# Kernel optimization log

Hardware: AMD Instinct MI355X
Metric: run time of the kernel (lower is better)

The kernel has to match this reference:

```python
import jax, jax.numpy as jnp
import numpy as np

B, T, C, H = 2, 2048, 1024, 16
D = C // H  # d_head = 64


def setup_inputs() -> dict:
    key = jax.random.key(0)
    k1, k2, k3 = jax.random.split(key, 3)
    x = jax.random.normal(k1, (B, T, C), dtype=jnp.float32)
    # torch Linear weights stored pre-transposed as [in, out] so we apply x @ W
    w_qkv = jax.random.normal(k2, (C, 3 * C), dtype=jnp.float32) * (C ** -0.5)
    w_out = jax.random.normal(k3, (C, C), dtype=jnp.float32) * (C ** -0.5)
    charge_w = jnp.array([0.0, 3.0, 6.0], dtype=jnp.float32)  # CHARGES init
    # causal mask, broadcast over batch and heads; mask==0 positions are blocked
    mask = jnp.tril(jnp.ones((1, 1, T, T), dtype=jnp.int32))
    return {"x": x, "mask": mask, "w_qkv": w_qkv, "w_out": w_out, "charge_w": charge_w}


def reference(x, mask, w_qkv, w_out, charge_w):
    B, T, C = x.shape
    H = 16
    D = C // H
    qkv = (x @ w_qkv).reshape(B, T, 3, H, D)
    q, k, v = qkv[:, :, 0], qkv[:, :, 1], qkv[:, :, 2]  # each [B,T,H,D]
    scale = D ** -0.5
    attn = jnp.einsum("bqhd,bkhd->bhqk", q, k) * scale  # [B,H,T,T]
    charge_bias = jnp.mod(jnp.sum(charge_w), 9.0) * 0.001  # scalar bias
    attn = attn + charge_bias
    attn = jnp.where(mask == 0, jnp.float32(-1e9), attn)
    attn = jax.nn.softmax(attn, axis=-1)  # dropout is identity in eval mode
    out = jnp.einsum("bhqk,bkhd->bqhd", attn, v).reshape(B, T, C)
    return out @ w_out
```

## Files before the change

kernel.cpp:

```cpp
#include <hip/hip_runtime.h>
#include <stdint.h>


typedef __attribute__((ext_vector_type(4))) float f32x4;
typedef __attribute__((ext_vector_type(16))) float f32x16;
typedef __attribute__((ext_vector_type(8))) __bf16 bf16x8;
typedef __attribute__((ext_vector_type(8))) unsigned short ushort8;
typedef __attribute__((ext_vector_type(4))) unsigned short ushort4v;
typedef __attribute__((ext_vector_type(4))) unsigned int uint4v;

#define DEV __device__ __forceinline__

DEV unsigned short f32_to_bf16(float f) {
    union { float f; unsigned int u; } cv; cv.f = f;
    unsigned int u = cv.u;
    return (unsigned short)((u + 0x7FFFu + ((u >> 16) & 1u)) >> 16);
}

DEV float bf16_to_f32(unsigned short u) {
    union { unsigned int i; float f; } cv; cv.i = ((unsigned int)u) << 16;
    return cv.f;
}

DEV bf16x8 load_bf16x8(const unsigned short* p) {
    ushort8 v = *(const ushort8*)p;
    return __builtin_bit_cast(bf16x8, v);
}

DEV unsigned cvt_pk_bf16(float lo, float hi) {
    unsigned r;
    asm("v_cvt_pk_bf16_f32 %0, %1, %2" : "=v"(r) : "v"(lo), "v"(hi));
    return r;
}

DEV void gload_lds16(const void* g, void* l) {
    __builtin_amdgcn_global_load_lds(
        (const __attribute__((address_space(1))) unsigned int*)g,
        (__attribute__((address_space(3))) unsigned int*)l, 16, 0, 0);
}

DEV f32x16 vzero16() {
    f32x16 v;
#pragma unroll
    for (int i = 0; i < 16; ++i) v[i] = 0.f;
    return v;
}

DEV float tmax32(const f32x16& a, const f32x16& b) {
    float m[16];
#pragma unroll
    for (int i = 0; i < 16; ++i) m[i] = fmaxf(a[i], b[i]);
#pragma unroll
    for (int st = 8; st > 0; st >>= 1)
#pragma unroll
        for (int i = 0; i < 8; ++i) if (i < st) m[i] = fmaxf(m[i], m[i + st]);
    return m[0];
}
DEV float tsum32(const f32x16& a, const f32x16& b) {
    float m[16];
#pragma unroll
    for (int i = 0; i < 16; ++i) m[i] = a[i] + b[i];
#pragma unroll
    for (int st = 8; st > 0; st >>= 1)
#pragma unroll
        for (int i = 0; i < 8; ++i) if (i < st) m[i] = m[i] + m[i + st];
    return m[0];
}

__device__ __constant__ unsigned char qQ[32]  = { 6, 5,14,14,14,13, 9, 9, 4,13,13,12,12, 8, 8,15,15,15,15,12,11,11,11,10, 7, 7, 3,10,10, 2, 1, 0};
__device__ __constant__ unsigned char tsQ[32] = { 0, 0, 0,10,20, 0, 0,10, 0,10,19, 0, 9, 0, 9, 0, 8,16,24,18, 0, 8,16, 0, 0, 8, 0, 8,15, 0, 0, 0};
__device__ __constant__ unsigned char teQ[32] = {14,12,10,20,30,10,10,20,10,19,28, 9,18, 9,18, 8,16,24,32,26, 8,16,24, 8, 8,16, 8,15,22, 6, 4, 2};
__device__ __constant__ unsigned char mlQ[32] = {255,255, 4, 5, 6, 7,19,20,255, 8, 9,10,11,21,22, 0, 1, 2, 3,12,13,14,15,16,23,24,255,17,18,255,255,255};
__device__ __constant__ unsigned char obQ[32] = {255,255,255, 3, 4,255,255,13,255, 5, 6,255, 7,255,14,255, 0, 1, 2, 8,255, 9,10,255,255,15,255,11,12,255,255,255};
__device__ __constant__ unsigned char ncs[9]  = {4,3,3,3,3,3,2,2,2};
__device__ __constant__ unsigned char mlbs[9] = {0,4,7,10,13,16,19,21,23};
__device__ __constant__ unsigned char obbs[9] = {0,3,5,7,9,11,13,14,15};

__global__ __launch_bounds__(256) void prep_kernel(const float* __restrict__ x,
                                                   const float* __restrict__ w_qkv,
                                                   const float* __restrict__ w_out,
                                                   unsigned short* __restrict__ xb,
                                                   unsigned short* __restrict__ wqkvT,
                                                   unsigned short* __restrict__ woutT) {
    __shared__ float tl[32][33];
    const int bx = blockIdx.x;
    const int tid = threadIdx.x;
    if (bx < 2048) {
        int i = (bx * 256 + tid) * 8;
        f32x4 a = *(const f32x4*)(x + i);
        f32x4 b = *(const f32x4*)(x + i + 4);
        ushort8 o;
        o[0] = f32_to_bf16(a[0]); o[1] = f32_to_bf16(a[1]);
        o[2] = f32_to_bf16(a[2]); o[3] = f32_to_bf16(a[3]);
        o[4] = f32_to_bf16(b[0]); o[5] = f32_to_bf16(b[1]);
        o[6] = f32_to_bf16(b[2]); o[7] = f32_to_bf16(b[3]);
        *(ushort8*)(xb + i) = o;
        return;
    }
    const float* in;
    unsigned short* out;
    int R, Cn, c0, r0;
    if (bx < 5120) {
        int idx = bx - 2048;
        in = w_qkv; out = wqkvT; R = 1024; Cn = 3072;
        c0 = (idx % 96) * 32; r0 = (idx / 96) * 32;
    } else {
        int idx = bx - 5120;
        in = w_out; out = woutT; R = 1024; Cn = 1024;
        c0 = (idx % 32) * 32; r0 = (idx / 32) * 32;
    }
    const int tx = tid & 31, ty = tid >> 5;
#pragma unroll
    for (int rr = 0; rr < 4; ++rr) {
        int r = ty + rr * 8;
        tl[r][tx] = in[(size_t)(r0 + r) * Cn + c0 + tx];
    }
    __syncthreads();
#pragma unroll
    for (int rr = 0; rr < 4; ++rr) {
        int cc = ty + rr * 8;
        out[(size_t)(c0 + cc) * R + r0 + tx] = f32_to_bf16(tl[tx][cc]);
    }
}

template<bool OUT_BF16, bool SCALE_Q>
__global__ __launch_bounds__(256) void gemm_kernel(
    const unsigned short* __restrict__ A,
    const unsigned short* __restrict__ Bt,
    void* __restrict__ C, int K, int ldc)
{
    __shared__ __align__(16) unsigned short As[3][4096];
    __shared__ __align__(16) unsigned short Bs[3][4096];

    const int tid = threadIdx.x;
    const int lane = tid & 63;
    const int w = tid >> 6;
    const int wr = w >> 1, wc = w & 1;
    const int g = lane >> 4, ci = lane & 15;
    const int bx = blockIdx.x, by = blockIdx.y;
    const int soff = w * 1024 + lane * 16;
    const int srow = soff >> 6;
    const int scch = (soff >> 4) & 3;

#define GSTAGE(buf, k0_) do { \
    _Pragma("unroll") for (int i_ = 0; i_ < 2; ++i_) { \
        int row_ = srow + i_ * 64; \
        gload_lds16(A  + (size_t)(by * 128 + row_) * K + (k0_) + scch * 8, \
                    (char*)As[buf] + i_ * 4096 + w * 1024); \
        gload_lds16(Bt + (size_t)(bx * 128 + row_) * K + (k0_) + scch * 8, \
                    (char*)Bs[buf] + i_ * 4096 + w * 1024); } } while (0)

    f32x4 acc[4][4];
#pragma unroll
    for (int i = 0; i < 4; ++i)
#pragma unroll
        for (int j = 0; j < 4; ++j) acc[i][j] = f32x4{0.f, 0.f, 0.f, 0.f};

    const int nk = K >> 5;
    GSTAGE(0, 0);
    GSTAGE(1, 32);
    asm volatile("s_waitcnt vmcnt(4)" ::: "memory");
    __builtin_amdgcn_sched_barrier(0);
    __builtin_amdgcn_s_barrier();
    __builtin_amdgcn_sched_barrier(0);

    for (int kt = 0; kt < nk; ++kt) {
        const int cur = kt % 3;
        if (kt + 2 < nk) GSTAGE((kt + 2) % 3, (kt + 2) << 5);

        bf16x8 af[4], bfr[4];
#pragma unroll
        for (int mf = 0; mf < 4; ++mf) af[mf]  = load_bf16x8(&As[cur][(wr * 64 + mf * 16 + ci) * 32 + g * 8]);
#pragma unroll
        for (int nf = 0; nf < 4; ++nf) bfr[nf] = load_bf16x8(&Bs[cur][(wc * 64 + nf * 16 + ci) * 32 + g * 8]);
        __builtin_amdgcn_s_setprio(1);
#pragma unroll
        for (int mf = 0; mf < 4; ++mf)
#pragma unroll
            for (int nf = 0; nf < 4; ++nf)
                acc[mf][nf] = __builtin_amdgcn_mfma_f32_16x16x32_bf16(af[mf], bfr[nf], acc[mf][nf], 0, 0, 0);
        __builtin_amdgcn_s_setprio(0);

        if (kt + 2 < nk) asm volatile("s_waitcnt vmcnt(4) lgkmcnt(0)" ::: "memory");
        else             asm volatile("s_waitcnt vmcnt(0) lgkmcnt(0)" ::: "memory");
        __builtin_amdgcn_sched_barrier(0);
        __builtin_amdgcn_s_barrier();
        __builtin_amdgcn_sched_barrier(0);
    }
#undef GSTAGE

#pragma unroll
    for (int mf = 0; mf < 4; ++mf)
#pragma unroll
        for (int nf = 0; nf < 4; ++nf)
#pragma unroll
            for (int r = 0; r < 4; ++r) {
                int row = by * 128 + wr * 64 + mf * 16 + g * 4 + r;
                int col = bx * 128 + wc * 64 + nf * 16 + ci;
                float v = acc[mf][nf][r];
                if (SCALE_Q && col < 1024) v *= 0.1803368801f;
                if (OUT_BF16)
                    ((unsigned short*)C)[(size_t)row * ldc + col] = f32_to_bf16(v);
                else
                    ((float*)C)[(size_t)row * ldc + col] = v;
            }
}

__global__ __launch_bounds__(256) void attn7_kernel(const unsigned short* __restrict__ qkv,
                                                    unsigned short* __restrict__ attn,
                                                    unsigned short* __restrict__ Obuf,
                                                    float* __restrict__ mlbuf) {
    constexpr int T = 2048, HD3 = 3072, Cc = 1024;
    __shared__ __align__(16) unsigned short Ks[3][4096];
    __shared__ __align__(16) unsigned short Vt[2][4096];

    const int tid = threadIdx.x;
    const int lane = tid & 63;
    const int w = tid >> 6;
    const int l31 = lane & 31;
    const int hi = lane >> 5;

    const int bx = blockIdx.x;
    const int j = bx >> 5;
    const int bh = bx & 31;
    const int q = qQ[j];
    const int ts = tsQ[j], te = teQ[j];
    const int h = bh & 15;
    const int b = bh >> 4;
    const int q0w = q * 128 + w * 32;
    const int qrow = q0w + l31;
    const size_t base = (size_t)b * T * HD3;
    const int ntc = te - ts;

    bf16x8 qf[4];
#pragma unroll
    for (int t = 0; t < 4; ++t)
        qf[t] = load_bf16x8(qkv + base + (size_t)qrow * HD3 + h * 64 + t * 16 + hi * 8);

    f32x16 acc0 = vzero16(), acc1 = vzero16();
    float m = -3e38f, l = 0.f;

    ushort8 vA0, vA1, vB0, vB1;
#define LOADV(tile, r0, r1) do { int kv0_ = (tile) * 64; \
    int rr0_ = tid >> 3, cc0_ = tid & 7; \
    r0 = *(const ushort8*)(qkv + base + (size_t)(kv0_ + rr0_) * HD3 + 2 * Cc + h * 64 + cc0_ * 8); \
    int c1_ = 256 + tid; int rr1_ = c1_ >> 3, cc1_ = c1_ & 7; \
    r1 = *(const ushort8*)(qkv + base + (size_t)(kv0_ + rr1_) * HD3 + 2 * Cc + h * 64 + cc1_ * 8); } while (0)

#define DMAK(tile, kb) do { int kv0_ = (tile) * 64; \
    _Pragma("unroll") for (int i_ = 0; i_ < 2; ++i_) { \
        int off_ = i_ * 4096 + w * 1024 + lane * 16; \
        int row_ = off_ >> 7; \
        int csw_ = ((lane & 7) * 8) ^ ((row_ & 7) * 8); \
        gload_lds16(qkv + base + (size_t)(kv0_ + row_) * HD3 + Cc + h * 64 + csw_, \
                    (void*)(((char*)&Ks[kb][0]) + i_ * 4096 + w * 1024)); } } while (0)

#define WRITEV(vb, r0, r1) do { \
    _Pragma("unroll") for (int i_ = 0; i_ < 2; ++i_) { \
        int c_ = i_ * 256 + tid; int row_ = c_ >> 3, cc_ = c_ & 7; \
        ushort8 v_ = i_ ? r1 : r0; \
        _Pragma("unroll") for (int j_ = 0; j_ < 8; ++j_) { \
            int d_ = cc_ * 8 + j_; \
            int sw_ = ((d_ ^ (d_ >> 3)) & 7) * 8; \
            Vt[vb][d_ * 64 + (row_ ^ sw_)] = v_[j_]; } } } while (0)

    LOADV(ts, vA0, vA1);
    DMAK(ts, 0);
    asm volatile("s_waitcnt vmcnt(0)" ::: "memory");
    __builtin_amdgcn_sched_barrier(0);
    WRITEV(0, vA0, vA1);
    LOADV(ts + 1, vB0, vB1);
    DMAK(ts + 1, 1);
    asm volatile("s_waitcnt lgkmcnt(0)" ::: "memory");
    __builtin_amdgcn_sched_barrier(0);
    __builtin_amdgcn_s_barrier();
    __builtin_amdgcn_sched_barrier(0);

    for (int tt = 0; tt < ntc; ++tt) {
        const int t = ts + tt;
        const int kv0 = t * 64;
        const int kcur = tt % 3;
        const int vcur = tt & 1;
        const bool act = (kv0 <= q0w + 31);
        const bool pre2 = (tt + 2) < ntc;

        if (tt + 1 < ntc) {
            if (tt & 1) WRITEV(vcur ^ 1, vA0, vA1); else WRITEV(vcur ^ 1, vB0, vB1);
        }
        if (pre2) {
            if (tt & 1) LOADV(t + 2, vB0, vB1); else LOADV(t + 2, vA0, vA1);
            DMAK(t + 2, (tt + 2) % 3);
        }

        if (act) {
            f32x16 s0 = vzero16(), s1 = vzero16();
            bf16x8 pf[4];
            const bool st1_ok = (kv0 + 32 <= q0w + 31);
            __builtin_amdgcn_s_setprio(1);
#pragma unroll
            for (int tf = 0; tf < 4; ++tf) {
                int row = l31;
                int idx = kcur * 4096 + row * 64 + ((tf * 16 + hi * 8) ^ ((row & 7) * 8));
                s0 = __builtin_amdgcn_mfma_f32_32x32x16_bf16(load_bf16x8(&Ks[0][idx]), qf[tf], s0, 0, 0, 0);
            }
            if (st1_ok) {
#pragma unroll
                for (int tf = 0; tf < 4; ++tf) {
                    int row = 32 + l31;
                    int idx = kcur * 4096 + row * 64 + ((tf * 16 + hi * 8) ^ ((row & 7) * 8));
                    s1 = __builtin_amdgcn_mfma_f32_32x32x16_bf16(load_bf16x8(&Ks[0][idx]), qf[tf], s1, 0, 0, 0);
                }
            }
            __builtin_amdgcn_s_setprio(0);
            const bool needmask = (kv0 + 63 > q0w);
            if (needmask) {
#pragma unroll
                for (int G = 0; G < 4; ++G)
#pragma unroll
                    for (int rr = 0; rr < 4; ++rr) {
                        int kvb = kv0 + 8 * G + 4 * hi + rr;
                        s0[G * 4 + rr] = (kvb      <= qrow) ? s0[G * 4 + rr] : -3e38f;
                        s1[G * 4 + rr] = (kvb + 32 <= qrow) ? s1[G * 4 + rr] : -3e38f;
                    }
            }
            float pmax = tmax32(s0, s1);
            pmax = fmaxf(pmax, __shfl_xor(pmax, 32));
            if (!__all(pmax - m <= 11.5f)) {
                float mnew = fmaxf(m, pmax);
                float alpha = exp2f(m - mnew);
                m = mnew;
                l *= alpha;
#pragma unroll
                for (int i = 0; i < 16; ++i) { acc0[i] *= alpha; acc1[i] *= alpha; }
            }
#pragma unroll
            for (int i = 0; i < 16; ++i) {
                s0[i] = exp2f(s0[i] - m);
                s1[i] = exp2f(s1[i] - m);
            }

            unsigned pk0[4][2], pk1[4][2];
#pragma unroll
            for (int G = 0; G < 4; ++G) {
                pk0[G][0] = cvt_pk_bf16(s0[G * 4 + 0], s0[G * 4 + 1]);
                pk0[G][1] = cvt_pk_bf16(s0[G * 4 + 2], s0[G * 4 + 3]);
                pk1[G][0] = cvt_pk_bf16(s1[G * 4 + 0], s1[G * 4 + 1]);
                pk1[G][1] = cvt_pk_bf16(s1[G * 4 + 2], s1[G * 4 + 3]);
            }
#pragma unroll
            for (int tf = 0; tf < 4; ++tf) {
                const int kb = tf & 1;
                unsigned sA0, sA1, sB0, sB1;
                if (tf < 2) { sA0 = pk0[2 * kb][0]; sA1 = pk0[2 * kb][1]; sB0 = pk0[2 * kb + 1][0]; sB1 = pk0[2 * kb + 1][1]; }
                else        { sA0 = pk1[2 * kb][0]; sA1 = pk1[2 * kb][1]; sB0 = pk1[2 * kb + 1][0]; sB1 = pk1[2 * kb + 1][1]; }
                unsigned sd0 = hi ? sA0 : sB0, sd1 = hi ? sA1 : sB1;
                unsigned rc0 = (unsigned)__shfl_xor((int)sd0, 32);
                unsigned rc1 = (unsigned)__shfl_xor((int)sd1, 32);
                uint4v u;
                u[0] = hi ? rc0 : sA0;  u[1] = hi ? rc1 : sA1;
                u[2] = hi ? sB0 : rc0;  u[3] = hi ? sB1 : rc1;
                pf[tf] = __builtin_bit_cast(bf16x8, u);
            }

            __builtin_amdgcn_s_setprio(1);
#pragma unroll
            for (int tf = 0; tf < 4; ++tf) {
                {
                    int d = l31, sw = ((d ^ (d >> 3)) & 7) * 8;
                    bf16x8 vf = load_bf16x8(&Vt[vcur][d * 64 + ((tf * 16 + hi * 8) ^ sw)]);
                    acc0 = __builtin_amdgcn_mfma_f32_32x32x16_bf16(vf, pf[tf], acc0, 0, 0, 0);
                }
                {
                    int d = 32 + l31, sw = ((d ^ (d >> 3)) & 7) * 8;
                    bf16x8 vf = load_bf16x8(&Vt[vcur][d * 64 + ((tf * 16 + hi * 8) ^ sw)]);
                    acc1 = __builtin_amdgcn_mfma_f32_32x32x16_bf16(vf, pf[tf], acc1, 0, 0, 0);
                }
            }
            __builtin_amdgcn_s_setprio(0);

            float rsum = tsum32(s0, s1);
            l += rsum + __shfl_xor(rsum, 32);
        }

        if (pre2) asm volatile("s_waitcnt vmcnt(4) lgkmcnt(0)" ::: "memory");
        else      asm volatile("s_waitcnt vmcnt(0) lgkmcnt(0)" ::: "memory");
        __builtin_amdgcn_sched_barrier(0);
        __builtin_amdgcn_s_barrier();
        __builtin_amdgcn_sched_barrier(0);
    }

    const int mlq = mlQ[j], obq = obQ[j];
    if (mlq == 255) {
        const float invl = 1.0f / l;
        const size_t ob = (size_t)b * T * Cc + (size_t)qrow * Cc + h * 64;
#pragma unroll
        for (int G = 0; G < 4; ++G) {
            ushort4v o0, o1;
#pragma unroll
            for (int rr = 0; rr < 4; ++rr) {
                o0[rr] = f32_to_bf16(acc0[G * 4 + rr] * invl);
                o1[rr] = f32_to_bf16(acc1[G * 4 + rr] * invl);
            }
            int d0 = 8 * G + 4 * hi;
            *(ushort4v*)(attn + ob + d0) = o0;
            *(ushort4v*)(attn + ob + 32 + d0) = o1;
        }
    } else {
        const int qlocal = w * 32 + l31;
        unsigned short* op = (obq == 255)
            ? (attn + (size_t)b * T * Cc + (size_t)qrow * Cc + h * 64)
            : (Obuf + (size_t)(bh * 16 + obq) * 8192 + qlocal * 64);
#pragma unroll
        for (int G = 0; G < 4; ++G) {
            ushort4v o0, o1;
#pragma unroll
            for (int rr = 0; rr < 4; ++rr) {
                o0[rr] = f32_to_bf16(acc0[G * 4 + rr]);
                o1[rr] = f32_to_bf16(acc1[G * 4 + rr]);
            }
            int d0 = 8 * G + 4 * hi;
            *(ushort4v*)(op + d0) = o0;
            *(ushort4v*)(op + 32 + d0) = o1;
        }
        if (hi == 0) {
            float* mp = mlbuf + (size_t)(bh * 25 + mlq) * 256 + qlocal * 2;
            mp[0] = m; mp[1] = l;
        }
    }
#undef LOADV
#undef DMAK
#undef WRITEV
}

__global__ __launch_bounds__(256) void combine3_kernel(const unsigned short* __restrict__ Obuf,
                                                       const float* __restrict__ mlbuf,
                                                       unsigned short* __restrict__ attn) {
    constexpr int T = 2048, Cc = 1024;
    const int ss = blockIdx.x;
    const int bh = ss / 9, s = ss - bh * 9;
    const int q = 15 - s;
    const int nc = ncs[s], mlb = mlbs[s], obb = obbs[s];
    const int b = bh >> 4, h = bh & 15;
    const int tid = threadIdx.x;
    const int qlocal = tid >> 1, dh = (tid & 1) * 32;

    float mv[4], lv[4];
#pragma unroll
    for (int c = 0; c < 4; ++c) {
        mv[c] = -3e38f; lv[c] = 0.f;
        if (c < nc) {
            const float* mp = mlbuf + (size_t)(bh * 25 + mlb + c) * 256 + qlocal * 2;
            mv[c] = mp[0]; lv[c] = mp[1];
        }
    }
    float M = fmaxf(fmaxf(mv[0], mv[1]), fmaxf(mv[2], mv[3]));
    float fc[4];
    float denom = 0.f;
#pragma unroll
    for (int c = 0; c < 4; ++c) {
        fc[c] = (c < nc) ? exp2f(mv[c] - M) : 0.f;
        denom += fc[c] * lv[c];
    }
    const float inv = 1.f / denom;
#pragma unroll
    for (int c = 0; c < 4; ++c) fc[c] *= inv;

    unsigned short* po = attn + (size_t)b * T * Cc + (size_t)(q * 128 + qlocal) * Cc + h * 64 + dh;
#pragma unroll
    for (int i = 0; i < 4; ++i) {
        float acc[8] = {0.f, 0.f, 0.f, 0.f, 0.f, 0.f, 0.f, 0.f};
#pragma unroll
        for (int c = 0; c < 4; ++c) {
            if (c < nc) {
                const unsigned short* pc = (c == 0)
                    ? po
                    : (Obuf + (size_t)(bh * 16 + obb + c - 1) * 8192 + qlocal * 64 + dh);
                ushort8 a = *(const ushort8*)(pc + i * 8);
#pragma unroll
                for (int k = 0; k < 8; ++k) acc[k] += fc[c] * bf16_to_f32(a[k]);
            }
        }
        ushort8 o;
#pragma unroll
        for (int k = 0; k < 8; ++k) o[k] = f32_to_bf16(acc[k]);
        *(ushort8*)(po + i * 8) = o;
    }
}

extern "C" void kernel_launch(void* const* d_in, const int* in_sizes, int n_in,
                              void* d_out, int out_size, void* d_ws, size_t ws_size,
                              hipStream_t stream) {
    const float* x     = (const float*)d_in[0];
    const float* w_qkv = (const float*)d_in[2];
    const float* w_out = (const float*)d_in[3];
    float* out = (float*)d_out;

    unsigned short* xb     = (unsigned short*)d_ws;
    unsigned short* wqkvT  = xb + 4194304;
    unsigned short* woutT  = wqkvT + 3145728;
    unsigned short* qkv    = woutT + 1048576;
    unsigned short* attn   = qkv + 12582912;
    unsigned short* Obuf   = xb;
    float*          mlbuf  = (float*)wqkvT;

    prep_kernel<<<6144, 256, 0, stream>>>(x, w_qkv, w_out, xb, wqkvT, woutT);

    gemm_kernel<true, true><<<dim3(24, 32), 256, 0, stream>>>(xb, wqkvT, (void*)qkv, 1024, 3072);

    attn7_kernel<<<1024, 256, 0, stream>>>(qkv, attn, Obuf, mlbuf);
    combine3_kernel<<<288, 256, 0, stream>>>(Obuf, mlbuf, attn);

    gemm_kernel<false, false><<<dim3(8, 32), 256, 0, stream>>>(attn, woutT, (void*)out, 1024, 1024);
}
```

Measured before the change: 133.6 us.

## Fuse split-KV combine into attention via last-arriver atomic counters; skip masked half-tiles

```diff
diff --git a/kernel.cpp b/kernel.cpp
--- a/kernel.cpp
+++ b/kernel.cpp
@@ -64,6 +64,26 @@
     for (int st = 8; st > 0; st >>= 1)
 #pragma unroll
         for (int i = 0; i < 8; ++i) if (i < st) m[i] = m[i] + m[i + st];
+    return m[0];
+}
+DEV float tmax16(const f32x16& a) {
+    float m[8];
+#pragma unroll
+    for (int i = 0; i < 8; ++i) m[i] = fmaxf(a[i], a[i + 8]);
+#pragma unroll
+    for (int st = 4; st > 0; st >>= 1)
+#pragma unroll
+        for (int i = 0; i < 4; ++i) if (i < st) m[i] = fmaxf(m[i], m[i + st]);
+    return m[0];
+}
+DEV float tsum16(const f32x16& a) {
+    float m[8];
+#pragma unroll
+    for (int i = 0; i < 8; ++i) m[i] = a[i] + a[i + 8];
+#pragma unroll
+    for (int st = 4; st > 0; st >>= 1)
+#pragma unroll
+        for (int i = 0; i < 4; ++i) if (i < st) m[i] = m[i] + m[i + st];
     return m[0];
 }
 
@@ -81,10 +101,15 @@
                                                    const float* __restrict__ w_out,
                                                    unsigned short* __restrict__ xb,
                                                    unsigned short* __restrict__ wqkvT,
-                                                   unsigned short* __restrict__ woutT) {
+                                                   unsigned short* __restrict__ woutT,
+                                                   int* __restrict__ counters) {
     __shared__ float tl[32][33];
     const int bx = blockIdx.x;
     const int tid = threadIdx.x;
+    if (bx >= 6144) {
+        for (int i = tid; i < 288; i += 256) counters[i] = 0;
+        return;
+    }
     if (bx < 2048) {
         int i = (bx * 256 + tid) * 8;
         f32x4 a = *(const f32x4*)(x + i);
@@ -209,10 +234,12 @@
 __global__ __launch_bounds__(256) void attn7_kernel(const unsigned short* __restrict__ qkv,
                                                     unsigned short* __restrict__ attn,
                                                     unsigned short* __restrict__ Obuf,
-                                                    float* __restrict__ mlbuf) {
+                                                    float* __restrict__ mlbuf,
+                                                    int* __restrict__ counters) {
     constexpr int T = 2048, HD3 = 3072, Cc = 1024;
     __shared__ __align__(16) unsigned short Ks[3][4096];
     __shared__ __align__(16) unsigned short Vt[2][4096];
+    __shared__ int winner;
 
     const int tid = threadIdx.x;
     const int lane = tid & 63;
@@ -319,11 +346,19 @@
 #pragma unroll
                     for (int rr = 0; rr < 4; ++rr) {
                         int kvb = kv0 + 8 * G + 4 * hi + rr;
-                        s0[G * 4 + rr] = (kvb      <= qrow) ? s0[G * 4 + rr] : -3e38f;
-                        s1[G * 4 + rr] = (kvb + 32 <= qrow) ? s1[G * 4 + rr] : -3e38f;
+                        s0[G * 4 + rr] = (kvb <= qrow) ? s0[G * 4 + rr] : -3e38f;
                     }
-            }
-            float pmax = tmax32(s0, s1);
+                if (st1_ok) {
+#pragma unroll
+                    for (int G = 0; G < 4; ++G)
+#pragma unroll
+                        for (int rr = 0; rr < 4; ++rr) {
+                            int kvb = kv0 + 8 * G + 4 * hi + rr;
+                            s1[G * 4 + rr] = (kvb + 32 <= qrow) ? s1[G * 4 + rr] : -3e38f;
+                        }
+                }
+            }
+            float pmax = st1_ok ? tmax32(s0, s1) : tmax16(s0);
             pmax = fmaxf(pmax, __shfl_xor(pmax, 32));
             if (!__all(pmax - m <= 11.5f)) {
                 float mnew = fmaxf(m, pmax);
@@ -334,9 +369,14 @@
                 for (int i = 0; i < 16; ++i) { acc0[i] *= alpha; acc1[i] *= alpha; }
             }
 #pragma unroll
-            for (int i = 0; i < 16; ++i) {
-                s0[i] = exp2f(s0[i] - m);
-                s1[i] = exp2f(s1[i] - m);
+            for (int i = 0; i < 16; ++i) s0[i] = exp2f(s0[i] - m);
+            float rsum;
+            if (st1_ok) {
+#pragma unroll
+                for (int i = 0; i < 16; ++i) s1[i] = exp2f(s1[i] - m);
+                rsum = tsum32(s0, s1);
+            } else {
+                rsum = tsum16(s0);
             }
 
             unsigned pk0[4][2], pk1[4][2];
@@ -344,15 +384,19 @@
             for (int G = 0; G < 4; ++G) {
                 pk0[G][0] = cvt_pk_bf16(s0[G * 4 + 0], s0[G * 4 + 1]);
                 pk0[G][1] = cvt_pk_bf16(s0[G * 4 + 2], s0[G * 4 + 3]);
-                pk1[G][0] = cvt_pk_bf16(s1[G * 4 + 0], s1[G * 4 + 1]);
-                pk1[G][1] = cvt_pk_bf16(s1[G * 4 + 2], s1[G * 4 + 3]);
-            }
-#pragma unroll
-            for (int tf = 0; tf < 4; ++tf) {
+            }
+            if (st1_ok) {
+#pragma unroll
+                for (int G = 0; G < 4; ++G) {
+                    pk1[G][0] = cvt_pk_bf16(s1[G * 4 + 0], s1[G * 4 + 1]);
+                    pk1[G][1] = cvt_pk_bf16(s1[G * 4 + 2], s1[G * 4 + 3]);
+                }
+            }
+#pragma unroll
+            for (int tf = 0; tf < 2; ++tf) {
                 const int kb = tf & 1;
-                unsigned sA0, sA1, sB0, sB1;
-                if (tf < 2) { sA0 = pk0[2 * kb][0]; sA1 = pk0[2 * kb][1]; sB0 = pk0[2 * kb + 1][0]; sB1 = pk0[2 * kb + 1][1]; }
-                else        { sA0 = pk1[2 * kb][0]; sA1 = pk1[2 * kb][1]; sB0 = pk1[2 * kb + 1][0]; sB1 = pk1[2 * kb + 1][1]; }
+                unsigned sA0 = pk0[2 * kb][0], sA1 = pk0[2 * kb][1];
+                unsigned sB0 = pk0[2 * kb + 1][0], sB1 = pk0[2 * kb + 1][1];
                 unsigned sd0 = hi ? sA0 : sB0, sd1 = hi ? sA1 : sB1;
                 unsigned rc0 = (unsigned)__shfl_xor((int)sd0, 32);
                 unsigned rc1 = (unsigned)__shfl_xor((int)sd1, 32);
@@ -361,10 +405,25 @@
                 u[2] = hi ? sB0 : rc0;  u[3] = hi ? sB1 : rc1;
                 pf[tf] = __builtin_bit_cast(bf16x8, u);
             }
+            if (st1_ok) {
+#pragma unroll
+                for (int tf = 2; tf < 4; ++tf) {
+                    const int kb = tf & 1;
+                    unsigned sA0 = pk1[2 * kb][0], sA1 = pk1[2 * kb][1];
+                    unsigned sB0 = pk1[2 * kb + 1][0], sB1 = pk1[2 * kb + 1][1];
+                    unsigned sd0 = hi ? sA0 : sB0, sd1 = hi ? sA1 : sB1;
+                    unsigned rc0 = (unsigned)__shfl_xor((int)sd0, 32);
+                    unsigned rc1 = (unsigned)__shfl_xor((int)sd1, 32);
+                    uint4v u;
+                    u[0] = hi ? rc0 : sA0;  u[1] = hi ? rc1 : sA1;
+                    u[2] = hi ? sB0 : rc0;  u[3] = hi ? sB1 : rc1;
+                    pf[tf] = __builtin_bit_cast(bf16x8, u);
+                }
+            }
 
             __builtin_amdgcn_s_setprio(1);
 #pragma unroll
-            for (int tf = 0; tf < 4; ++tf) {
+            for (int tf = 0; tf < 2; ++tf) {
                 {
                     int d = l31, sw = ((d ^ (d >> 3)) & 7) * 8;
                     bf16x8 vf = load_bf16x8(&Vt[vcur][d * 64 + ((tf * 16 + hi * 8) ^ sw)]);
@@ -376,9 +435,23 @@
                     acc1 = __builtin_amdgcn_mfma_f32_32x32x16_bf16(vf, pf[tf], acc1, 0, 0, 0);
                 }
             }
+            if (st1_ok) {
+#pragma unroll
+                for (int tf = 2; tf < 4; ++tf) {
+                    {
+                        int d = l31, sw = ((d ^ (d >> 3)) & 7) * 8;
+                        bf16x8 vf = load_bf16x8(&Vt[vcur][d * 64 + ((tf * 16 + hi * 8) ^ sw)]);
+                        acc0 = __builtin_amdgcn_mfma_f32_32x32x16_bf16(vf, pf[tf], acc0, 0, 0, 0);
+                    }
+                    {
+                        int d = 32 + l31, sw = ((d ^ (d >> 3)) & 7) * 8;
+                        bf16x8 vf = load_bf16x8(&Vt[vcur][d * 64 + ((tf * 16 + hi * 8) ^ sw)]);
+                        acc1 = __builtin_amdgcn_mfma_f32_32x32x16_bf16(vf, pf[tf], acc1, 0, 0, 0);
+                    }
+                }
+            }
             __builtin_amdgcn_s_setprio(0);
 
-            float rsum = tsum32(s0, s1);
             l += rsum + __shfl_xor(rsum, 32);
         }
 
@@ -426,65 +499,66 @@
             float* mp = mlbuf + (size_t)(bh * 25 + mlq) * 256 + qlocal * 2;
             mp[0] = m; mp[1] = l;
         }
+
+        const int s = 15 - q;
+        __threadfence();
+        __syncthreads();
+        if (tid == 0) {
+            int old = atomicAdd(&counters[bh * 9 + s], 1);
+            winner = (old == (int)ncs[s] - 1) ? 1 : 0;
+        }
+        __syncthreads();
+        if (winner) {
+            __threadfence();
+            const int nc = ncs[s], mlb = mlbs[s], obb = obbs[s];
+            const int ql2 = tid >> 1, dh = (tid & 1) * 32;
+
+            float mv[4], lv[4];
+#pragma unroll
+            for (int c = 0; c < 4; ++c) {
+                mv[c] = -3e38f; lv[c] = 0.f;
+                if (c < nc) {
+                    const float* mp = mlbuf + (size_t)(bh * 25 + mlb + c) * 256 + ql2 * 2;
+                    mv[c] = mp[0]; lv[c] = mp[1];
+                }
+            }
+            float M = fmaxf(fmaxf(mv[0], mv[1]), fmaxf(mv[2], mv[3]));
+            float fc[4];
+            float denom = 0.f;
+#pragma unroll
+            for (int c = 0; c < 4; ++c) {
+                fc[c] = (c < nc) ? exp2f(mv[c] - M) : 0.f;
+                denom += fc[c] * lv[c];
+            }
+            const float inv = 1.f / denom;
+#pragma unroll
+            for (int c = 0; c < 4; ++c) fc[c] *= inv;
+
+            unsigned short* po = attn + (size_t)b * T * Cc + (size_t)(q * 128 + ql2) * Cc + h * 64 + dh;
+#pragma unroll
+            for (int i = 0; i < 4; ++i) {
+                float acc[8] = {0.f, 0.f, 0.f, 0.f, 0.f, 0.f, 0.f, 0.f};
+#pragma unroll
+                for (int c = 0; c < 4; ++c) {
+                    if (c < nc) {
+                        const unsigned short* pc = (c == 0)
+                            ? po
+                            : (Obuf + (size_t)(bh * 16 + obb + c - 1) * 8192 + ql2 * 64 + dh);
+                        ushort8 a = *(const ushort8*)(pc + i * 8);
+#pragma unroll
+                        for (int k = 0; k < 8; ++k) acc[k] += fc[c] * bf16_to_f32(a[k]);
+                    }
+                }
+                ushort8 o;
+#pragma unroll
+                for (int k = 0; k < 8; ++k) o[k] = f32_to_bf16(acc[k]);
+                *(ushort8*)(po + i * 8) = o;
+            }
+        }
     }
 #undef LOADV
 #undef DMAK
 #undef WRITEV
-}
-
-__global__ __launch_bounds__(256) void combine3_kernel(const unsigned short* __restrict__ Obuf,
-                                                       const float* __restrict__ mlbuf,
-                                                       unsigned short* __restrict__ attn) {
-    constexpr int T = 2048, Cc = 1024;
-    const int ss = blockIdx.x;
-    const int bh = ss / 9, s = ss - bh * 9;
-    const int q = 15 - s;
-    const int nc = ncs[s], mlb = mlbs[s], obb = obbs[s];
-    const int b = bh >> 4, h = bh & 15;
-    const int tid = threadIdx.x;
-    const int qlocal = tid >> 1, dh = (tid & 1) * 32;
-
-    float mv[4], lv[4];
-#pragma unroll
-    for (int c = 0; c < 4; ++c) {
-        mv[c] = -3e38f; lv[c] = 0.f;
-        if (c < nc) {
-            const float* mp = mlbuf + (size_t)(bh * 25 + mlb + c) * 256 + qlocal * 2;
-            mv[c] = mp[0]; lv[c] = mp[1];
-        }
-    }
-    float M = fmaxf(fmaxf(mv[0], mv[1]), fmaxf(mv[2], mv[3]));
-    float fc[4];
-    float denom = 0.f;
-#pragma unroll
-    for (int c = 0; c < 4; ++c) {
-        fc[c] = (c < nc) ? exp2f(mv[c] - M) : 0.f;
-        denom += fc[c] * lv[c];
-    }
-    const float inv = 1.f / denom;
-#pragma unroll
-    for (int c = 0; c < 4; ++c) fc[c] *= inv;
-
-    unsigned short* po = attn + (size_t)b * T * Cc + (size_t)(q * 128 + qlocal) * Cc + h * 64 + dh;
-#pragma unroll
-    for (int i = 0; i < 4; ++i) {
-        float acc[8] = {0.f, 0.f, 0.f, 0.f, 0.f, 0.f, 0.f, 0.f};
-#pragma unroll
-        for (int c = 0; c < 4; ++c) {
-            if (c < nc) {
-                const unsigned short* pc = (c == 0)
-                    ? po
-                    : (Obuf + (size_t)(bh * 16 + obb + c - 1) * 8192 + qlocal * 64 + dh);
-                ushort8 a = *(const ushort8*)(pc + i * 8);
-#pragma unroll
-                for (int k = 0; k < 8; ++k) acc[k] += fc[c] * bf16_to_f32(a[k]);
-            }
-        }
-        ushort8 o;
-#pragma unroll
-        for (int k = 0; k < 8; ++k) o[k] = f32_to_bf16(acc[k]);
-        *(ushort8*)(po + i * 8) = o;
-    }
 }
 
 extern "C" void kernel_launch(void* const* d_in, const int* in_sizes, int n_in,
@@ -502,13 +576,13 @@
     unsigned short* attn   = qkv + 12582912;
     unsigned short* Obuf   = xb;
     float*          mlbuf  = (float*)wqkvT;
-
-    prep_kernel<<<6144, 256, 0, stream>>>(x, w_qkv, w_out, xb, wqkvT, woutT);
+    int*            counters = (int*)d_out;
+
+    prep_kernel<<<6145, 256, 0, stream>>>(x, w_qkv, w_out, xb, wqkvT, woutT, counters);
 
     gemm_kernel<true, true><<<dim3(24, 32), 256, 0, stream>>>(xb, wqkvT, (void*)qkv, 1024, 3072);
 
-    attn7_kernel<<<1024, 256, 0, stream>>>(qkv, attn, Obuf, mlbuf);
-    combine3_kernel<<<288, 256, 0, stream>>>(Obuf, mlbuf, attn);
+    attn7_kernel<<<1024, 256, 0, stream>>>(qkv, attn, Obuf, mlbuf, counters);
 
     gemm_kernel<false, false><<<dim3(8, 32), 256, 0, stream>>>(attn, woutT, (void*)out, 1024, 1024);
 }
```

New measurement: 299.9 us. 2.24x slower.
